# Kernel optimization log

Measured on AMD Instinct MI355X. Metric: run time of the kernel, lower is better.

The kernel has to match this reference:

```python
import jax, jax.numpy as jnp
import numpy as np

EMBED_SIZE = 1024
HEADS = 16
HEAD_DIM = EMBED_SIZE // HEADS
NEG_INF = -1e20


def setup_inputs() -> dict:
    key = jax.random.key(0)
    k1, k2, k3, k4, k5, k6, k7 = jax.random.split(key, 7)
    N, S = 2, 2048
    values = jax.random.normal(k1, (N, S, EMBED_SIZE), dtype=jnp.float32)
    keys = jax.random.normal(k2, (N, S, EMBED_SIZE), dtype=jnp.float32)
    query = jax.random.normal(k3, (N, S, EMBED_SIZE), dtype=jnp.float32)
    mask = jnp.ones((N, 1, S, S), dtype=bool)
    # Per-head projection weights (shared across heads), torch Linear convention y = x @ W.T
    sc = 1.0 / np.sqrt(HEAD_DIM)
    Wq = jax.random.uniform(k4, (HEAD_DIM, HEAD_DIM), jnp.float32, -sc, sc)
    Wk = jax.random.uniform(k5, (HEAD_DIM, HEAD_DIM), jnp.float32, -sc, sc)
    Wv = jax.random.uniform(k6, (HEAD_DIM, HEAD_DIM), jnp.float32, -sc, sc)
    sco = 1.0 / np.sqrt(EMBED_SIZE)
    k7a, k7b = jax.random.split(k7)
    Wo = jax.random.uniform(k7a, (EMBED_SIZE, EMBED_SIZE), jnp.float32, -sco, sco)
    bo = jax.random.uniform(k7b, (EMBED_SIZE,), jnp.float32, -sco, sco)
    return {"values": values, "keys": keys, "query": query, "mask": mask,
            "Wq": Wq, "Wk": Wk, "Wv": Wv, "Wo": Wo, "bo": bo}


def reference(values, keys, query, mask, Wq, Wk, Wv, Wo, bo):
    N, Q, E = query.shape
    K = keys.shape[1]
    H, D = HEADS, HEAD_DIM
    v = values.reshape(N, K, H, D)
    k = keys.reshape(N, K, H, D)
    q = query.reshape(N, Q, H, D)
    # per-head linear (weights shared across heads): y = x @ W.T
    q = jnp.einsum('nqhd,ed->nqhe', q, Wq)
    k = jnp.einsum('nkhd,ed->nkhe', k, Wk)
    v = jnp.einsum('nkhd,ed->nkhe', v, Wv)
    energy = jnp.einsum('nqhd,nkhd->nhqk', q, k)  # [N,H,Q,K]
    energy = jnp.where(mask, energy, NEG_INF)
    # NOTE: original scales by sqrt(embed_size), not sqrt(head_dim)
    attn = jax.nn.softmax(energy / (E ** 0.5), axis=-1)
    out = jnp.einsum('nhqk,nkhd->nqhd', attn, v).reshape(N, Q, H * D)
    return out @ Wo.T + bo
```

## Files before the change

kernel.cpp:

```cpp
#include <hip/hip_runtime.h>
#include <hip/hip_bf16.h>


typedef __bf16 bf16_t;
typedef __bf16 bf16x4_t __attribute__((ext_vector_type(4)));
typedef __bf16 bf16x8_t __attribute__((ext_vector_type(8)));
typedef float f32x4_t __attribute__((ext_vector_type(4)));
typedef float f32x16_t __attribute__((ext_vector_type(16)));

#define MFMA16(a, b, c) __builtin_amdgcn_mfma_f32_16x16x32_bf16((a), (b), (c), 0, 0, 0)
#define MFMA32(a, b, c) __builtin_amdgcn_mfma_f32_32x32x16_bf16((a), (b), (c), 0, 0, 0)

static __device__ __forceinline__ bf16x8_t cvt8(float4 a, float4 b) {
  bf16x8_t r = { (bf16_t)a.x, (bf16_t)a.y, (bf16_t)a.z, (bf16_t)a.w,
                 (bf16_t)b.x, (bf16_t)b.y, (bf16_t)b.z, (bf16_t)b.w };
  return r;
}

static __device__ __forceinline__ unsigned pack2(float a, float b) {
  union { bf16_t h[2]; unsigned u; } x;
  x.h[0] = (bf16_t)a; x.h[1] = (bf16_t)b;
  return x.u;
}

__global__ __launch_bounds__(256) void k_cvt_wo(const float* __restrict__ w,
                                                bf16_t* __restrict__ o) {
  int i = (blockIdx.x * 256 + threadIdx.x) * 4;
  float4 v = *(const float4*)(w + i);
  bf16x4_t r = { (bf16_t)v.x, (bf16_t)v.y, (bf16_t)v.z, (bf16_t)v.w };
  *(bf16x4_t*)(o + i) = r;
}

__global__ __launch_bounds__(256) void k_tilemask(const int* __restrict__ mask32,
                                                  unsigned char* __restrict__ tm) {
  const int b = blockIdx.x;
  const int n = b >> 10, qt = (b >> 5) & 31, kt = b & 31;
  const int t = threadIdx.x;
  const int row = t >> 2;
  const int mtype = (mask32[0] == 1);
  bool ok;
  if (mtype) {
    const uint4* base = (const uint4*)(mask32 + (size_t)n * 4194304 +
                                       (size_t)(qt * 64 + row) * 2048 + kt * 64);
    ok = true;
    #pragma unroll
    for (int j = 0; j < 4; ++j) {
      uint4 v = base[(t & 3) * 4 + j];
      ok = ok && v.x && v.y && v.z && v.w;
    }
  } else {
    const unsigned char* maskb = (const unsigned char*)mask32;
    const int c = (t & 3) * 16;
    uint4 v = *(const uint4*)(maskb + (size_t)n * 4194304 +
                              (size_t)(qt * 64 + row) * 2048 + kt * 64 + c);
    ok = ((v.x & v.y & v.z & v.w) == 0x01010101u);
  }
  __shared__ int ok_s;
  if (t == 0) ok_s = 1;
  __syncthreads();
  if (!ok) atomicAnd(&ok_s, 0);
  __syncthreads();
  if (t == 0) tm[b] = (unsigned char)ok_s;
}

__global__ __launch_bounds__(256) void k_proj_qk(const float* __restrict__ x,
                                                 const float* __restrict__ w,
                                                 bf16_t* __restrict__ out, float oscale) {
  __shared__ __align__(16) ushort Xs[256 * 64];
  const int t = threadIdx.x;
  const int r0 = blockIdx.x * 256;
  const int lane = t & 63, wv = t >> 6;
  const int g = lane >> 4, l15 = lane & 15;
  #pragma unroll
  for (int i = 0; i < 16; ++i) {
    int c = t + 256 * i;
    float4 v = *(const float4*)(x + (size_t)r0 * 64 + (size_t)c * 4);
    int row = c >> 4;
    int off = ((c & 15) * 8) ^ ((row & 7) << 4);
    bf16x4_t bv = { (bf16_t)v.x, (bf16_t)v.y, (bf16_t)v.z, (bf16_t)v.w };
    *(bf16x4_t*)((char*)Xs + row * 128 + off) = bv;
  }
  bf16x8_t bw[4][2];
  #pragma unroll
  for (int nf = 0; nf < 4; ++nf)
    #pragma unroll
    for (int ks = 0; ks < 2; ++ks) {
      const float* wp = w + (nf * 16 + l15) * 64 + ks * 32 + g * 8;
      bw[nf][ks] = cvt8(*(const float4*)wp, *(const float4*)(wp + 4));
    }
  __syncthreads();
  f32x4_t acc[4][4] = {};
  #pragma unroll
  for (int mi = 0; mi < 4; ++mi) {
    int row = wv * 64 + mi * 16 + l15;
    int sw = (row & 7) << 4;
    bf16x8_t a0 = *(const bf16x8_t*)((char*)Xs + row * 128 + ((g * 16) ^ sw));
    bf16x8_t a1 = *(const bf16x8_t*)((char*)Xs + row * 128 + ((64 + g * 16) ^ sw));
    #pragma unroll
    for (int nf = 0; nf < 4; ++nf) {
      acc[mi][nf] = MFMA16(a0, bw[nf][0], acc[mi][nf]);
      acc[mi][nf] = MFMA16(a1, bw[nf][1], acc[mi][nf]);
    }
  }
  #pragma unroll
  for (int mi = 0; mi < 4; ++mi)
    #pragma unroll
    for (int rr = 0; rr < 4; ++rr) {
      int r = r0 + wv * 64 + mi * 16 + g * 4 + rr;
      int h = r & 15, s = (r >> 4) & 2047, n = r >> 15;
      bf16_t* op = out + ((size_t)(n * 16 + h) * 2048 + s) * 64;
      #pragma unroll
      for (int nf = 0; nf < 4; ++nf)
        op[nf * 16 + l15] = (bf16_t)(acc[mi][nf][rr] * oscale);
    }
}

__global__ __launch_bounds__(256) void k_proj_v(const float* __restrict__ x,
                                                const float* __restrict__ w,
                                                bf16_t* __restrict__ vt) {
  const int b = blockIdx.x;
  const int sb = b & 7, nh = b >> 3;
  const int h = nh & 15, n = nh >> 4;
  const int t = threadIdx.x, lane = t & 63, wv = t >> 6;
  const int g = lane >> 4, l15 = lane & 15;
  const int s0 = sb * 256 + wv * 64;
  bf16x8_t bx[4][2];
  #pragma unroll
  for (int ni = 0; ni < 4; ++ni)
    #pragma unroll
    for (int ks = 0; ks < 2; ++ks) {
      int s = s0 + ni * 16 + l15;
      const float* xp = x + ((size_t)n * 2048 + s) * 1024 + h * 64 + ks * 32 + g * 8;
      bx[ni][ks] = cvt8(*(const float4*)xp, *(const float4*)(xp + 4));
    }
  f32x4_t acc[4][4] = {};
  #pragma unroll
  for (int mi = 0; mi < 4; ++mi) {
    const float* wp = w + (mi * 16 + l15) * 64 + g * 8;
    bf16x8_t a0 = cvt8(*(const float4*)wp, *(const float4*)(wp + 4));
    bf16x8_t a1 = cvt8(*(const float4*)(wp + 32), *(const float4*)(wp + 36));
    #pragma unroll
    for (int ni = 0; ni < 4; ++ni) {
      acc[mi][ni] = MFMA16(a0, bx[ni][0], acc[mi][ni]);
      acc[mi][ni] = MFMA16(a1, bx[ni][1], acc[mi][ni]);
    }
  }
  #pragma unroll
  for (int mi = 0; mi < 4; ++mi)
    #pragma unroll
    for (int rr = 0; rr < 4; ++rr) {
      int d = mi * 16 + g * 4 + rr;
      bf16_t* vp = vt + ((size_t)nh * 64 + d) * 2048 + s0;
      #pragma unroll
      for (int ni = 0; ni < 4; ++ni)
        vp[ni * 16 + l15] = (bf16_t)acc[mi][ni][rr];
    }
}

__global__ __launch_bounds__(256, 2) void k_attn(const bf16_t* __restrict__ Qp,
                                                 const bf16_t* __restrict__ Kp,
                                                 const bf16_t* __restrict__ VT,
                                                 const int* __restrict__ mask32,
                                                 const unsigned char* __restrict__ tm,
                                                 bf16_t* __restrict__ ao) {
  __shared__ __align__(128) char lds[32768];
  const int bid = blockIdx.x;
  const int w = ((bid & 7) << 6) + (bid >> 3);
  const int qb = w & 15, nh = w >> 4;
  const int n = nh >> 4, h = nh & 15;
  const int t = threadIdx.x, lane = t & 63, wv = t >> 6;
  const int l31 = lane & 31, hi = lane >> 5;
  const int q0w = qb * 128 + wv * 32;
  const size_t kvbase = (size_t)nh * (2048 * 64);
  const int mtype = (mask32[0] == 1);

  bf16x8_t qf[4];
  #pragma unroll
  for (int kd = 0; kd < 4; ++kd)
    qf[kd] = *(const bf16x8_t*)(Qp + kvbase + (size_t)(q0w + l31) * 64 + kd * 16 + hi * 8);

  f32x16_t o0 = {}, o1 = {};
  float l_r = 0.f;

  const unsigned char* tmrow = tm + ((size_t)n * 32 + (q0w >> 6)) * 32;
  const int soff = ((lane & 7) << 4) ^ ((lane >> 3) << 4);
  const char* gK = (const char*)(Kp + kvbase);
  const char* gV = (const char*)(VT + kvbase);

#define STAGE(ktile, bufsel)                                                          \
  do {                                                                                \
    const int kb_ = (ktile) * 64;                                                     \
    _Pragma("unroll")                                                                 \
    for (int i_ = 0; i_ < 2; ++i_) {                                                  \
      const int row_ = wv * 16 + i_ * 8 + (lane >> 3);                                \
      char* dst_ = lds + (bufsel) * 16384 + wv * 2048 + i_ * 1024;                    \
      __builtin_amdgcn_global_load_lds(                                               \
          (const __attribute__((address_space(1))) void*)(gK + (size_t)(kb_ + row_) * 128 + soff), \
          (__attribute__((address_space(3))) void*)dst_, 16, 0, 0);                   \
      __builtin_amdgcn_global_load_lds(                                               \
          (const __attribute__((address_space(1))) void*)(gV + (size_t)row_ * 4096 + (size_t)kb_ * 2 + soff), \
          (__attribute__((address_space(3))) void*)(dst_ + 8192), 16, 0, 0);          \
    }                                                                                 \
  } while (0)

  int buf = 0;
  STAGE(0, 0);
  asm volatile("s_waitcnt vmcnt(0)" ::: "memory");
  __syncthreads();

  for (int kt = 0; kt < 32; ++kt) {
    if (kt < 31) STAGE(kt + 1, buf ^ 1);
    const char* Ksb = lds + buf * 16384;
    const char* Vsb = Ksb + 8192;
    const int rsw = (l31 & 7) << 4;

    f32x16_t s0 = {}, s1 = {};
    __builtin_amdgcn_s_setprio(1);
    #pragma unroll
    for (int kd = 0; kd < 4; ++kd) {
      int off = kd * 32 + hi * 16;
      bf16x8_t k0 = *(const bf16x8_t*)(Ksb + l31 * 128 + (off ^ rsw));
      bf16x8_t k1 = *(const bf16x8_t*)(Ksb + (32 + l31) * 128 + (off ^ rsw));
      s0 = MFMA32(k0, qf[kd], s0);
      s1 = MFMA32(k1, qf[kd], s1);
    }
    __builtin_amdgcn_s_setprio(0);

    if (!tmrow[kt]) {
      #pragma unroll
      for (int r = 0; r < 16; ++r) {
        int krow = (r & 3) + 8 * (r >> 2) + 4 * hi;
        size_t base = (size_t)n * 4194304 + (size_t)(q0w + l31) * 2048 + kt * 64 + krow;
        bool m0 = mtype ? (mask32[base] != 0) : (((const unsigned char*)mask32)[base] != 0);
        bool m1 = mtype ? (mask32[base + 32] != 0) : (((const unsigned char*)mask32)[base + 32] != 0);
        if (!m0) s0[r] = -1.0e19f;
        if (!m1) s1[r] = -1.0e19f;
      }
    }

    float rs = 0.f;
    #pragma unroll
    for (int r = 0; r < 16; ++r) { float p = __builtin_exp2f(s0[r]); s0[r] = p; rs += p; }
    #pragma unroll
    for (int r = 0; r < 16; ++r) { float p = __builtin_exp2f(s1[r]); s1[r] = p; rs += p; }
    l_r += rs;

    unsigned pk0[4][2], pk1[4][2];
    #pragma unroll
    for (int rq = 0; rq < 4; ++rq)
      #pragma unroll
      for (int ww = 0; ww < 2; ++ww) {
        pk0[rq][ww] = pack2(s0[4 * rq + 2 * ww], s0[4 * rq + 2 * ww + 1]);
        pk1[rq][ww] = pack2(s1[4 * rq + 2 * ww], s1[4 * rq + 2 * ww + 1]);
      }
    bf16x8_t paf[4];
    #pragma unroll
    for (int tt = 0; tt < 2; ++tt)
      #pragma unroll
      for (int k2 = 0; k2 < 2; ++k2) {
        unsigned a0 = tt ? pk1[2 * k2][0] : pk0[2 * k2][0];
        unsigned a1 = tt ? pk1[2 * k2][1] : pk0[2 * k2][1];
        unsigned b0 = tt ? pk1[2 * k2 + 1][0] : pk0[2 * k2 + 1][0];
        unsigned b1 = tt ? pk1[2 * k2 + 1][1] : pk0[2 * k2 + 1][1];
        unsigned sa0 = __shfl_xor(a0, 32), sa1 = __shfl_xor(a1, 32);
        unsigned sb0 = __shfl_xor(b0, 32), sb1 = __shfl_xor(b1, 32);
        union { unsigned u[4]; bf16x8_t v; } f;
        f.u[0] = hi ? sb0 : a0;
        f.u[1] = hi ? sb1 : a1;
        f.u[2] = hi ? b0 : sa0;
        f.u[3] = hi ? b1 : sa1;
        paf[tt * 2 + k2] = f.v;
      }

    __builtin_amdgcn_s_setprio(1);
    #pragma unroll
    for (int ks = 0; ks < 4; ++ks) {
      int off = ks * 32 + hi * 16;
      bf16x8_t v0 = *(const bf16x8_t*)(Vsb + l31 * 128 + (off ^ rsw));
      bf16x8_t v1 = *(const bf16x8_t*)(Vsb + (32 + l31) * 128 + (off ^ rsw));
      o0 = MFMA32(v0, paf[ks], o0);
      o1 = MFMA32(v1, paf[ks], o1);
    }
    __builtin_amdgcn_s_setprio(0);

    asm volatile("s_waitcnt vmcnt(0)" ::: "memory");
    __syncthreads();
    buf ^= 1;
  }
#undef STAGE

  l_r += __shfl_xor(l_r, 32);
  float inv = 1.f / fmaxf(l_r, 1e-37f);
  bf16_t* op = ao + ((size_t)n * 2048 + q0w + l31) * 1024 + h * 64;
  #pragma unroll
  for (int rq = 0; rq < 4; ++rq) {
    bf16x4_t w0, w1;
    #pragma unroll
    for (int e = 0; e < 4; ++e) {
      w0[e] = (bf16_t)(o0[4 * rq + e] * inv);
      w1[e] = (bf16_t)(o1[4 * rq + e] * inv);
    }
    *(bf16x4_t*)(op + 8 * rq + 4 * hi) = w0;
    *(bf16x4_t*)(op + 32 + 8 * rq + 4 * hi) = w1;
  }
}

__global__ __launch_bounds__(256, 2) void k_gemm_out(const bf16_t* __restrict__ A,
                                                     const bf16_t* __restrict__ B,
                                                     const float* __restrict__ bias,
                                                     float* __restrict__ C) {
  __shared__ __align__(128) char lds[65536];
  const int bid = blockIdx.x;
  const int w = ((bid & 7) << 5) + (bid >> 3);
  const int mb = w >> 3, nb = w & 7;
  const int m0 = mb * 128, n0 = nb * 128;
  const int t = threadIdx.x, lane = t & 63, wv = t >> 6;
  const int g = lane >> 4, l15 = lane & 15;
  const int wm = (wv >> 1) * 64, wn = (wv & 1) * 64;
  const int soff = ((lane & 7) << 4) ^ ((lane >> 3) << 4);
  const char* gA = (const char*)A;
  const char* gB = (const char*)B;

#define GSTAGE(k0_, bufsel)                                                           \
  do {                                                                                \
    _Pragma("unroll")                                                                 \
    for (int i_ = 0; i_ < 4; ++i_) {                                                  \
      const int row_ = wv * 32 + i_ * 8 + (lane >> 3);                                \
      char* dst_ = lds + (bufsel) * 32768 + wv * 4096 + i_ * 1024;                    \
      __builtin_amdgcn_global_load_lds(                                               \
          (const __attribute__((address_space(1))) void*)(gA + (size_t)(m0 + row_) * 2048 + (k0_) * 2 + soff), \
          (__attribute__((address_space(3))) void*)dst_, 16, 0, 0);                   \
      __builtin_amdgcn_global_load_lds(                                               \
          (const __attribute__((address_space(1))) void*)(gB + (size_t)(n0 + row_) * 2048 + (k0_) * 2 + soff), \
          (__attribute__((address_space(3))) void*)(dst_ + 16384), 16, 0, 0);         \
    }                                                                                 \
  } while (0)

  f32x4_t acc[4][4] = {};
  int buf = 0;
  GSTAGE(0, 0);
  asm volatile("s_waitcnt vmcnt(0)" ::: "memory");
  __syncthreads();

  for (int s = 0; s < 16; ++s) {
    if (s < 15) GSTAGE((s + 1) * 64, buf ^ 1);
    const char* As = lds + buf * 32768;
    const char* Bs = As + 16384;
    bf16x8_t af[4][2], bfr[4][2];
    #pragma unroll
    for (int mi = 0; mi < 4; ++mi) {
      int row = wm + mi * 16 + l15;
      int sw = (row & 7) << 4;
      af[mi][0] = *(const bf16x8_t*)(As + row * 128 + ((g * 16) ^ sw));
      af[mi][1] = *(const bf16x8_t*)(As + row * 128 + ((64 + g * 16) ^ sw));
    }
    #pragma unroll
    for (int ni = 0; ni < 4; ++ni) {
      int row = wn + ni * 16 + l15;
      int sw = (row & 7) << 4;
      bfr[ni][0] = *(const bf16x8_t*)(Bs + row * 128 + ((g * 16) ^ sw));
      bfr[ni][1] = *(const bf16x8_t*)(Bs + row * 128 + ((64 + g * 16) ^ sw));
    }
    __builtin_amdgcn_s_setprio(1);
    #pragma unroll
    for (int mi = 0; mi < 4; ++mi)
      #pragma unroll
      for (int ni = 0; ni < 4; ++ni) {
        acc[mi][ni] = MFMA16(af[mi][0], bfr[ni][0], acc[mi][ni]);
        acc[mi][ni] = MFMA16(af[mi][1], bfr[ni][1], acc[mi][ni]);
      }
    __builtin_amdgcn_s_setprio(0);
    asm volatile("s_waitcnt vmcnt(0)" ::: "memory");
    __syncthreads();
    buf ^= 1;
  }
#undef GSTAGE

  float bv[4];
  #pragma unroll
  for (int ni = 0; ni < 4; ++ni) bv[ni] = bias[n0 + wn + ni * 16 + l15];
  #pragma unroll
  for (int mi = 0; mi < 4; ++mi)
    #pragma unroll
    for (int rr = 0; rr < 4; ++rr) {
      int row = m0 + wm + mi * 16 + g * 4 + rr;
      float* cp = C + (size_t)row * 1024 + n0 + wn;
      #pragma unroll
      for (int ni = 0; ni < 4; ++ni)
        cp[ni * 16 + l15] = acc[mi][ni][rr] + bv[ni];
    }
}

extern "C" void kernel_launch(void* const* d_in, const int* in_sizes, int n_in,
                              void* d_out, int out_size, void* d_ws, size_t ws_size,
                              hipStream_t stream) {
  (void)in_sizes; (void)n_in; (void)out_size; (void)ws_size;
  const float* values = (const float*)d_in[0];
  const float* keys   = (const float*)d_in[1];
  const float* query  = (const float*)d_in[2];
  const int*   mask   = (const int*)d_in[3];
  const float* Wq = (const float*)d_in[4];
  const float* Wk = (const float*)d_in[5];
  const float* Wv = (const float*)d_in[6];
  const float* Wo = (const float*)d_in[7];
  const float* bo = (const float*)d_in[8];
  float* out = (float*)d_out;

  char* ws = (char*)d_ws;
  bf16_t* Qp  = (bf16_t*)(ws);
  bf16_t* Kp  = (bf16_t*)(ws + (8u << 20));
  bf16_t* VTp = (bf16_t*)(ws + (16u << 20));
  bf16_t* AO  = (bf16_t*)(ws + (24u << 20));
  bf16_t* WOb = (bf16_t*)(ws + (32u << 20));
  unsigned char* TM = (unsigned char*)(ws + (34u << 20));

  k_cvt_wo<<<dim3(1024), dim3(256), 0, stream>>>(Wo, WOb);
  k_tilemask<<<dim3(2048), dim3(256), 0, stream>>>(mask, TM);
  k_proj_qk<<<dim3(256), dim3(256), 0, stream>>>(query, Wq, Qp, 0.045084220027885f);
  k_proj_qk<<<dim3(256), dim3(256), 0, stream>>>(keys, Wk, Kp, 1.0f);
  k_proj_v<<<dim3(256), dim3(256), 0, stream>>>(values, Wv, VTp);
  k_attn<<<dim3(512), dim3(256), 0, stream>>>(Qp, Kp, VTp, mask, TM, AO);
  k_gemm_out<<<dim3(256), dim3(256), 0, stream>>>(AO, WOb, bo, out);
}
```

Baseline: 251.0 us.

## Triple-buffer attention KV staging, coalesce V projection via LDS, use permlane32 swap

The attention kernel moves from double to triple buffering of K/V tiles. It prefetches two tiles ahead and waits with a partial vmcnt, so loads overlap more compute, at the cost of more LDS per block and possibly fewer resident blocks. The V projection now stages the whole 256-row input tile through swizzled LDS with coalesced loads instead of per-lane strided reads. Separately, the cross-half shuffle of the probability fragments uses v_permlane32_swap instead of four shfl_xor plus selects, and all s_setprio hints are removed.

```diff
diff --git a/kernel.cpp b/kernel.cpp
--- a/kernel.cpp
+++ b/kernel.cpp
@@ -118,42 +118,53 @@
 __global__ __launch_bounds__(256) void k_proj_v(const float* __restrict__ x,
                                                 const float* __restrict__ w,
                                                 bf16_t* __restrict__ vt) {
+  __shared__ __align__(16) ushort Xs[256 * 64];
   const int b = blockIdx.x;
   const int sb = b & 7, nh = b >> 3;
   const int h = nh & 15, n = nh >> 4;
   const int t = threadIdx.x, lane = t & 63, wv = t >> 6;
   const int g = lane >> 4, l15 = lane & 15;
-  const int s0 = sb * 256 + wv * 64;
-  bf16x8_t bx[4][2];
-  #pragma unroll
-  for (int ni = 0; ni < 4; ++ni)
+  const int s0b = sb * 256;
+  #pragma unroll
+  for (int i = 0; i < 16; ++i) {
+    int c = t + 256 * i;
+    int row = c >> 4, off16 = c & 15;
+    float4 v = *(const float4*)(x + ((size_t)n * 2048 + s0b + row) * 1024 + h * 64 + off16 * 4);
+    int off = (off16 * 8) ^ ((row & 7) << 4);
+    bf16x4_t bv = { (bf16_t)v.x, (bf16_t)v.y, (bf16_t)v.z, (bf16_t)v.w };
+    *(bf16x4_t*)((char*)Xs + row * 128 + off) = bv;
+  }
+  bf16x8_t aw[4][2];
+  #pragma unroll
+  for (int dt = 0; dt < 4; ++dt)
     #pragma unroll
     for (int ks = 0; ks < 2; ++ks) {
-      int s = s0 + ni * 16 + l15;
-      const float* xp = x + ((size_t)n * 2048 + s) * 1024 + h * 64 + ks * 32 + g * 8;
-      bx[ni][ks] = cvt8(*(const float4*)xp, *(const float4*)(xp + 4));
-    }
+      const float* wp = w + (dt * 16 + l15) * 64 + ks * 32 + g * 8;
+      aw[dt][ks] = cvt8(*(const float4*)wp, *(const float4*)(wp + 4));
+    }
+  __syncthreads();
   f32x4_t acc[4][4] = {};
   #pragma unroll
-  for (int mi = 0; mi < 4; ++mi) {
-    const float* wp = w + (mi * 16 + l15) * 64 + g * 8;
-    bf16x8_t a0 = cvt8(*(const float4*)wp, *(const float4*)(wp + 4));
-    bf16x8_t a1 = cvt8(*(const float4*)(wp + 32), *(const float4*)(wp + 36));
-    #pragma unroll
-    for (int ni = 0; ni < 4; ++ni) {
-      acc[mi][ni] = MFMA16(a0, bx[ni][0], acc[mi][ni]);
-      acc[mi][ni] = MFMA16(a1, bx[ni][1], acc[mi][ni]);
-    }
-  }
-  #pragma unroll
-  for (int mi = 0; mi < 4; ++mi)
+  for (int st = 0; st < 4; ++st) {
+    int row = wv * 64 + st * 16 + l15;
+    int sw = (row & 7) << 4;
+    bf16x8_t b0 = *(const bf16x8_t*)((char*)Xs + row * 128 + ((g * 16) ^ sw));
+    bf16x8_t b1 = *(const bf16x8_t*)((char*)Xs + row * 128 + ((64 + g * 16) ^ sw));
+    #pragma unroll
+    for (int dt = 0; dt < 4; ++dt) {
+      acc[dt][st] = MFMA16(aw[dt][0], b0, acc[dt][st]);
+      acc[dt][st] = MFMA16(aw[dt][1], b1, acc[dt][st]);
+    }
+  }
+  #pragma unroll
+  for (int dt = 0; dt < 4; ++dt)
     #pragma unroll
     for (int rr = 0; rr < 4; ++rr) {
-      int d = mi * 16 + g * 4 + rr;
-      bf16_t* vp = vt + ((size_t)nh * 64 + d) * 2048 + s0;
-      #pragma unroll
-      for (int ni = 0; ni < 4; ++ni)
-        vp[ni * 16 + l15] = (bf16_t)acc[mi][ni][rr];
+      int d = dt * 16 + g * 4 + rr;
+      bf16_t* vp = vt + ((size_t)nh * 64 + d) * 2048 + s0b + wv * 64;
+      #pragma unroll
+      for (int st = 0; st < 4; ++st)
+        vp[st * 16 + l15] = (bf16_t)acc[dt][st][rr];
     }
 }
 
@@ -163,7 +174,7 @@
                                                  const int* __restrict__ mask32,
                                                  const unsigned char* __restrict__ tm,
                                                  bf16_t* __restrict__ ao) {
-  __shared__ __align__(128) char lds[32768];
+  __shared__ __align__(128) char lds[49152];
   const int bid = blockIdx.x;
   const int w = ((bid & 7) << 6) + (bid >> 3);
   const int qb = w & 15, nh = w >> 4;
@@ -203,19 +214,19 @@
     }                                                                                 \
   } while (0)
 
-  int buf = 0;
   STAGE(0, 0);
-  asm volatile("s_waitcnt vmcnt(0)" ::: "memory");
-  __syncthreads();
-
+  STAGE(1, 1);
+  asm volatile("s_waitcnt vmcnt(4)" ::: "memory");
+  __builtin_amdgcn_s_barrier();
+
+  int cur = 0, pre = 2;
   for (int kt = 0; kt < 32; ++kt) {
-    if (kt < 31) STAGE(kt + 1, buf ^ 1);
-    const char* Ksb = lds + buf * 16384;
+    if (kt < 30) STAGE(kt + 2, pre);
+    const char* Ksb = lds + cur * 16384;
     const char* Vsb = Ksb + 8192;
     const int rsw = (l31 & 7) << 4;
 
     f32x16_t s0 = {}, s1 = {};
-    __builtin_amdgcn_s_setprio(1);
     #pragma unroll
     for (int kd = 0; kd < 4; ++kd) {
       int off = kd * 32 + hi * 16;
@@ -224,7 +235,6 @@
       s0 = MFMA32(k0, qf[kd], s0);
       s1 = MFMA32(k1, qf[kd], s1);
     }
-    __builtin_amdgcn_s_setprio(0);
 
     if (!tmrow[kt]) {
       #pragma unroll
@@ -262,17 +272,13 @@
         unsigned a1 = tt ? pk1[2 * k2][1] : pk0[2 * k2][1];
         unsigned b0 = tt ? pk1[2 * k2 + 1][0] : pk0[2 * k2 + 1][0];
         unsigned b1 = tt ? pk1[2 * k2 + 1][1] : pk0[2 * k2 + 1][1];
-        unsigned sa0 = __shfl_xor(a0, 32), sa1 = __shfl_xor(a1, 32);
-        unsigned sb0 = __shfl_xor(b0, 32), sb1 = __shfl_xor(b1, 32);
+        asm("v_permlane32_swap_b32 %0, %1" : "+v"(a0), "+v"(b0));
+        asm("v_permlane32_swap_b32 %0, %1" : "+v"(a1), "+v"(b1));
         union { unsigned u[4]; bf16x8_t v; } f;
-        f.u[0] = hi ? sb0 : a0;
-        f.u[1] = hi ? sb1 : a1;
-        f.u[2] = hi ? b0 : sa0;
-        f.u[3] = hi ? b1 : sa1;
+        f.u[0] = a0; f.u[1] = a1; f.u[2] = b0; f.u[3] = b1;
         paf[tt * 2 + k2] = f.v;
       }
 
-    __builtin_amdgcn_s_setprio(1);
     #pragma unroll
     for (int ks = 0; ks < 4; ++ks) {
       int off = ks * 32 + hi * 16;
@@ -281,11 +287,12 @@
       o0 = MFMA32(v0, paf[ks], o0);
       o1 = MFMA32(v1, paf[ks], o1);
     }
-    __builtin_amdgcn_s_setprio(0);
-
-    asm volatile("s_waitcnt vmcnt(0)" ::: "memory");
-    __syncthreads();
-    buf ^= 1;
+
+    if (kt < 30) asm volatile("s_waitcnt vmcnt(4) lgkmcnt(0)" ::: "memory");
+    else         asm volatile("s_waitcnt vmcnt(0) lgkmcnt(0)" ::: "memory");
+    __builtin_amdgcn_s_barrier();
+    cur = (cur == 2) ? 0 : cur + 1;
+    pre = (pre == 2) ? 0 : pre + 1;
   }
 #undef STAGE
 
@@ -361,7 +368,6 @@
       bfr[ni][0] = *(const bf16x8_t*)(Bs + row * 128 + ((g * 16) ^ sw));
       bfr[ni][1] = *(const bf16x8_t*)(Bs + row * 128 + ((64 + g * 16) ^ sw));
     }
-    __builtin_amdgcn_s_setprio(1);
     #pragma unroll
     for (int mi = 0; mi < 4; ++mi)
       #pragma unroll
@@ -369,7 +375,6 @@
         acc[mi][ni] = MFMA16(af[mi][0], bfr[ni][0], acc[mi][ni]);
         acc[mi][ni] = MFMA16(af[mi][1], bfr[ni][1], acc[mi][ni]);
       }
-    __builtin_amdgcn_s_setprio(0);
     asm volatile("s_waitcnt vmcnt(0)" ::: "memory");
     __syncthreads();
     buf ^= 1;
```

Measured after the change: 249.4 us. About the same (-0.6%).
